# Optimization experiments

Hardware: AMD Instinct MI355X
Metric: run time of the kernel (lower is better)

The kernel has to match this reference:

```python
import jax, jax.numpy as jnp
import numpy as np
from jax import lax

B, T = 128, 512
V, D = 100000, 100   # word vocab, word embedding dim
H = 100              # per-direction LSTM hidden (concat -> 200)
L = 25               # number of CRF labels


def setup_inputs() -> dict:
    key = jax.random.key(0)
    ks = jax.random.split(key, 16)
    s = 0.02
    inp = {
        "tok_tensor": jax.random.randint(ks[0], (B, T), 0, V, dtype=jnp.int32),
        "tag_tensor": jax.random.randint(ks[1], (B, T), 0, L, dtype=jnp.int32),
        "lengths": jnp.full((B,), T, dtype=jnp.int32),
        "word_emb": jax.random.normal(ks[2], (V, D), jnp.float32) * s,
        # forward-direction LSTM (PyTorch gate order i,f,g,o)
        "w_ih_f": jax.random.normal(ks[3], (4 * H, D), jnp.float32) * s,
        "w_hh_f": jax.random.normal(ks[4], (4 * H, H), jnp.float32) * s,
        "b_ih_f": jax.random.normal(ks[5], (4 * H,), jnp.float32) * s,
        "b_hh_f": jax.random.normal(ks[6], (4 * H,), jnp.float32) * s,
        # backward-direction LSTM
        "w_ih_b": jax.random.normal(ks[7], (4 * H, D), jnp.float32) * s,
        "w_hh_b": jax.random.normal(ks[8], (4 * H, H), jnp.float32) * s,
        "b_ih_b": jax.random.normal(ks[9], (4 * H,), jnp.float32) * s,
        "b_hh_b": jax.random.normal(ks[10], (4 * H,), jnp.float32) * s,
        # hidden2tag linear
        "w_tag": jax.random.normal(ks[11], (L, 2 * H), jnp.float32) * s,
        "b_tag": jax.random.normal(ks[12], (L,), jnp.float32) * s,
        # CRF params
        "transitions": jax.random.normal(ks[13], (L, L), jnp.float32) * 0.1,
        "start_trans": jax.random.normal(ks[14], (L,), jnp.float32) * 0.1,
        "end_trans": jax.random.normal(ks[15], (L,), jnp.float32) * 0.1,
    }
    return inp


def _lstm(x_tbd, w_ih, w_hh, b_ih, b_hh, reverse):
    """x_tbd: [T,B,D] -> hidden states [T,B,H], aligned with input time axis."""
    Bh = x_tbd.shape[1]
    Hh = w_hh.shape[1]
    h0 = jnp.zeros((Bh, Hh), x_tbd.dtype)
    c0 = jnp.zeros((Bh, Hh), x_tbd.dtype)

    def step(carry, xt):
        h, c = carry
        gates = xt @ w_ih.T + b_ih + h @ w_hh.T + b_hh
        i, f, g, o = jnp.split(gates, 4, axis=-1)
        i = jax.nn.sigmoid(i); f = jax.nn.sigmoid(f)
        g = jnp.tanh(g); o = jax.nn.sigmoid(o)
        c = f * c + i * g
        h = o * jnp.tanh(c)
        return (h, c), h

    _, hs = lax.scan(step, (h0, c0), x_tbd, reverse=reverse)
    return hs


def _crf_nll(emissions, tags, mask, transitions, start_trans, end_trans):
    """Sum over batch of -(gold path score - log partition).
    emissions: [B,T,L], tags: [B,T] int, mask: [B,T] float (1=valid)."""
    Bb = emissions.shape[0]
    b_idx = jnp.arange(Bb)
    em_t = emissions.transpose(1, 0, 2)   # [T,B,L]
    tags_t = tags.T                       # [T,B]
    mask_t = mask.T                       # [T,B]

    # --- gold path score ---
    first_tags = tags_t[0]
    score0 = start_trans[first_tags] + em_t[0][b_idx, first_tags]

    def num_step(score, inp):
        em, tp, tc, m = inp  # emissions[t], tags[t-1], tags[t], mask[t]
        s = transitions[tp, tc] + em[b_idx, tc]
        return score + m * s, None

    gold, _ = lax.scan(num_step, score0,
                       (em_t[1:], tags_t[:-1], tags_t[1:], mask_t[1:]))
    last_idx = jnp.sum(mask, axis=1).astype(jnp.int32) - 1
    last_tags = tags[b_idx, last_idx]
    gold = gold + end_trans[last_tags]

    # --- log partition (forward algorithm) ---
    alpha0 = start_trans + em_t[0]  # [B,L]

    def part_step(alpha, inp):
        em, m = inp
        # [B,L_prev,1] + [L_prev,L_next] + [B,1,L_next]
        nxt = jax.nn.logsumexp(alpha[:, :, None] + transitions[None] + em[:, None, :], axis=1)
        alpha = jnp.where(m[:, None] > 0, nxt, alpha)
        return alpha, None

    alpha, _ = lax.scan(part_step, alpha0, (em_t[1:], mask_t[1:]))
    logZ = jax.nn.logsumexp(alpha + end_trans, axis=1)
    return jnp.sum(logZ - gold)


def reference(tok_tensor, tag_tensor, lengths,
              word_emb, w_ih_f, w_hh_f, b_ih_f, b_hh_f,
              w_ih_b, w_hh_b, b_ih_b, b_hh_b,
              w_tag, b_tag, transitions, start_trans, end_trans):
    # word embedding lookup: [B,T,D]
    tok_embs = word_emb[tok_tensor]
    x_tbd = tok_embs.transpose(1, 0, 2)  # [T,B,D]
    # BiLSTM encoder (dropout off: eval / deterministic reference)
    h_fwd = _lstm(x_tbd, w_ih_f, w_hh_f, b_ih_f, b_hh_f, reverse=False)
    h_bwd = _lstm(x_tbd, w_ih_b, w_hh_b, b_ih_b, b_hh_b, reverse=True)
    seq = jnp.concatenate([h_fwd, h_bwd], axis=-1).transpose(1, 0, 2)  # [B,T,2H]
    # hidden2tag
    emissions = jnp.einsum('btd,ld->btl', seq, w_tag) + b_tag  # [B,T,L]
    # CRF negative log-likelihood
    mask = (jnp.arange(T)[None, :] < lengths[:, None]).astype(emissions.dtype)
    return _crf_nll(emissions, tag_tensor, mask, transitions, start_trans, end_trans)
```

## Files before the change

kernel.cpp:

```cpp
#include <hip/hip_runtime.h>
#include <cstdint>
#include <cstddef>

#define BB 128
#define TT 512
#define DD 100
#define HH 100
#define NG 400
#define LL 25
#define TS 32
#define NTILE 16
#define F_LOG2E 1.44269504088896340736f
#define F_LN2   0.69314718055994530942f

typedef __decltype(__builtin_amdgcn_cvt_pkrtz(0.f, 0.f)) h2_t;
typedef _Float16 v8h __attribute__((ext_vector_type(8)));
typedef float v4f __attribute__((ext_vector_type(4)));

__device__ __forceinline__ h2_t bc_h2(unsigned int u) {
  return __builtin_bit_cast(h2_t, u);
}
__device__ __forceinline__ unsigned int pk(float x, float y) {
  return __builtin_bit_cast(unsigned int, __builtin_amdgcn_cvt_pkrtz(x, y));
}

__device__ __forceinline__ float fdot2(h2_t a, h2_t b, float c) {
#if __has_builtin(__builtin_amdgcn_fdot2)
  return __builtin_amdgcn_fdot2(a, b, c, false);
#else
  return c + (float)a[0] * (float)b[0] + (float)a[1] * (float)b[1];
#endif
}

__device__ __forceinline__ float fexp2(float x) { return __builtin_amdgcn_exp2f(x); }
__device__ __forceinline__ float flog2(float x) { return __builtin_amdgcn_logf(x); }
__device__ __forceinline__ float frcp(float x)  { return __builtin_amdgcn_rcpf(x); }

__device__ __forceinline__ float sigmoid_f(float x) {
  return frcp(1.f + fexp2(-F_LOG2E * x));
}
__device__ __forceinline__ float tanh_f(float x) {
  float e = fexp2(2.f * F_LOG2E * x);
  return 1.f - 2.f * frcp(e + 1.f);
}

template <int CTRL>
__device__ __forceinline__ float qadd(float v) {
#if __has_builtin(__builtin_amdgcn_mov_dpp)
  int m = __builtin_amdgcn_mov_dpp(__builtin_bit_cast(int, v), CTRL, 0xF, 0xF, true);
  return v + __builtin_bit_cast(float, m);
#else
  int x = (CTRL == 177) ? 1 : 2;
  return v + __shfl_xor(v, x);
#endif
}

template <int LANE>
__device__ __forceinline__ float qbcast(float v) {
#if __has_builtin(__builtin_amdgcn_mov_dpp)
  int m = __builtin_amdgcn_mov_dpp(__builtin_bit_cast(int, v), LANE * 0x55, 0xF, 0xF, true);
  return __builtin_bit_cast(float, m);
#else
  return __shfl(v, (threadIdx.x & 63 & ~3) + LANE);
#endif
}

__device__ __forceinline__ float rfl(float v) {
  return __builtin_bit_cast(float,
      __builtin_amdgcn_readfirstlane(__builtin_bit_cast(int, v)));
}

__device__ __forceinline__ void wave_fence() {
#if __has_builtin(__builtin_amdgcn_wave_barrier)
  __builtin_amdgcn_wave_barrier();
#endif
}

__device__ __forceinline__ void lds_barrier() {
  __builtin_amdgcn_s_waitcnt(0xC07F);
  __builtin_amdgcn_s_barrier();
}

__global__ __launch_bounds__(512, 2) void lstm_fused3(
    const int* __restrict__ tok, const float* __restrict__ emb,
    const float* __restrict__ w_ih_f, const float* __restrict__ w_ih_b,
    const float* __restrict__ b_ih_f, const float* __restrict__ b_hh_f,
    const float* __restrict__ b_ih_b, const float* __restrict__ b_hh_b,
    const float* __restrict__ w_hh_f, const float* __restrict__ w_hh_b,
    const float* __restrict__ w_tag, const float* __restrict__ b_tag,
    float* __restrict__ em_f, float* __restrict__ em_b)
{
  const int tid = threadIdx.x;
  const int b   = blockIdx.x & 127;
  const int dir = blockIdx.x >> 7;
  const float* w_hh = dir ? w_hh_b : w_hh_f;
  const float* w_ih = dir ? w_ih_b : w_ih_f;
  const float* b_ih = dir ? b_ih_b : b_ih_f;
  const float* b_hh = dir ? b_hh_b : b_hh_f;

  __shared__ __align__(16) unsigned short gin_lds[TS * 400];
  __shared__ __align__(16) unsigned int xlds[TS * 68];
  __shared__ __align__(16) unsigned int hls0[52];
  __shared__ __align__(16) unsigned int hls1[52];

  const int wv   = tid >> 6;
  const int lane = tid & 63;
  const int l16  = lane & 15;
  const int quad = lane >> 4;
  const int c0b  = (25 * wv) >> 3;
  const int c1b  = (25 * (wv + 1)) >> 3;
  const int ncol = c1b - c0b;

  v8h bfr[4][4];
  int pcol[4];
#pragma unroll
  for (int ci = 0; ci < 4; ++ci) {
    const int cc = (ci < ncol) ? (c0b + ci) : c0b;
    const int n  = 16 * cc + l16;
    const float* wr = w_ih + (size_t)n * DD;
#pragma unroll
    for (int f = 0; f < 3; ++f) {
      const float* wp = wr + f * 32 + quad * 8;
      float4 va = *(const float4*)(wp);
      float4 vb = *(const float4*)(wp + 4);
      uint4 u;
      u.x = pk(va.x, va.y); u.y = pk(va.z, va.w);
      u.z = pk(vb.x, vb.y); u.w = pk(vb.z, vb.w);
      bfr[ci][f] = __builtin_bit_cast(v8h, u);
    }
    {
      uint4 u = {0u, 0u, 0u, 0u};
      if (quad == 0) {
        float4 va = *(const float4*)(wr + 96);
        u.x = pk(va.x, va.y); u.y = pk(va.z, va.w);
      }
      bfr[ci][3] = __builtin_bit_cast(v8h, u);
    }
    const int qn = (n * 41) >> 12;
    pcol[ci] = ((n - 100 * qn) << 2) + qn;
  }

  for (int i = tid; i < TS * 18; i += 512) {
    int row = i / 18;
    int d = i - row * 18;
    xlds[row * 68 + 50 + d] = 0u;
  }

  const bool uact = tid < NG;
  const int j = tid >> 2;
  const int s = tid & 3;
  const int od = 12 * s;
  const int nnv = (s == 3) ? 14 : 12;

  h2_t wA[14], wB[14], wC[14], wD[14];
  float bias = 0.f;
  if (uact) {
#pragma unroll
    for (int d = 0; d < 14; ++d) {
      int dd = (d < nnv) ? (od + d) : 0;
      const float* r0 = w_hh + (size_t)(0 * 100 + j) * HH + 2 * dd;
      const float* r1 = w_hh + (size_t)(1 * 100 + j) * HH + 2 * dd;
      const float* r2 = w_hh + (size_t)(2 * 100 + j) * HH + 2 * dd;
      const float* r3 = w_hh + (size_t)(3 * 100 + j) * HH + 2 * dd;
      h2_t z = __builtin_amdgcn_cvt_pkrtz(0.f, 0.f);
      wA[d] = (d < nnv) ? __builtin_amdgcn_cvt_pkrtz(r0[0], r0[1]) : z;
      wB[d] = (d < nnv) ? __builtin_amdgcn_cvt_pkrtz(r1[0], r1[1]) : z;
      wC[d] = (d < nnv) ? __builtin_amdgcn_cvt_pkrtz(r2[0], r2[1]) : z;
      wD[d] = (d < nnv) ? __builtin_amdgcn_cvt_pkrtz(r3[0], r3[1]) : z;
    }
    bias = b_ih[s * 100 + j] + b_hh[s * 100 + j];
  }
  const float kk2 = (s == 2) ? (2.f * F_LOG2E) : (-F_LOG2E);
  const float cA  = (s == 2) ? -2.f : 1.f;
  const float cB  = (s == 2) ? 1.f : 0.f;

  const int el = tid - 448;
  const bool eact = (el >= 0) && (el < 50);
  const int l  = (el >= 0) ? (el >> 1) : 0;
  const int hf = (el >= 0) ? (el & 1) : 0;
  const int eo = hf ? 24 : 0;
  const int en = hf ? 26 : 24;
  h2_t wt[26];
  float bt = 0.f;
  if (eact) {
    const float* wr = w_tag + (size_t)l * 200 + dir * 100;
#pragma unroll
    for (int d = 0; d < 26; ++d) {
      int dd = (d < en) ? (eo + d) : 0;
      h2_t z = __builtin_amdgcn_cvt_pkrtz(0.f, 0.f);
      wt[d] = (d < en) ? __builtin_amdgcn_cvt_pkrtz(wr[2 * dd], wr[2 * dd + 1]) : z;
    }
    if (dir == 0 && hf == 0) bt = b_tag[l];
  }
  float* emo = dir ? em_b : em_f;
  float* emp = emo + ((size_t)b * TT + (dir ? (TT - 1) : 0)) * LL + l;
  const ptrdiff_t estep = dir ? -(ptrdiff_t)LL : (ptrdiff_t)LL;

  if (tid < 52) { hls0[tid] = 0u; hls1[tid] = 0u; }

  const int tprow = tid / 13;
  const int tps   = tid - 13 * tprow;
  const bool tp_act = tid < 416;

  float4 xa = {0, 0, 0, 0}, xb = {0, 0, 0, 0};
  if (tp_act) {
    int ii = tprow;
    int tt = dir ? (TT - 1 - ii) : ii;
    int tk = tok[b * TT + tt];
    const float* xp = emb + (size_t)tk * DD + 8 * tps;
    xa = *(const float4*)xp;
    if (tps < 12) xb = *(const float4*)(xp + 4);
  }

  float c = 0.f;
  unsigned short gnext = 0;
  int grow = 0;

#define SDOT(d, hh) \
  p0 = fdot2(wA[d], bc_h2(hh), p0); p1 = fdot2(wB[d], bc_h2(hh), p1); \
  p2 = fdot2(wC[d], bc_h2(hh), p2); p3 = fdot2(wD[d], bc_h2(hh), p3);
#define EDOT(d, hh) { h2_t h = bc_h2(hh); \
  if ((d & 3) == 0) a0 = fdot2(wt[d], h, a0); \
  else if ((d & 3) == 1) a1 = fdot2(wt[d], h, a1); \
  else if ((d & 3) == 2) a2 = fdot2(wt[d], h, a2); \
  else a3 = fdot2(wt[d], h, a3); }

#define SCAN_STEP(HRD, HWR, TVNZ)                                          \
  {                                                                        \
    if (uact) {                                                            \
      unsigned short gcurr = gnext;                                        \
      int nr = (grow < TS - 1) ? grow + 1 : TS - 1;                        \
      gnext = gin_lds[nr * 400 + tid];                                     \
      grow = nr;                                                           \
      const unsigned int* hp = (HRD) + od;                                 \
      uint4 u0 = *((const uint4*)hp);                                      \
      uint4 u1 = *((const uint4*)(hp + 4));                                \
      uint4 u2 = *((const uint4*)(hp + 8));                                \
      uint2 u3 = *((const uint2*)(hp + 12));                               \
      float p0, p1, p2, p3;                                                \
      p0 = fdot2(wA[0], bc_h2(u0.x), 0.f);                                 \
      p1 = fdot2(wB[0], bc_h2(u0.x), 0.f);                                 \
      p2 = fdot2(wC[0], bc_h2(u0.x), 0.f);                                 \
      p3 = fdot2(wD[0], bc_h2(u0.x), 0.f);                                 \
      SDOT(1, u0.y)  SDOT(2, u0.z)  SDOT(3, u0.w)                          \
      SDOT(4, u1.x)  SDOT(5, u1.y)  SDOT(6, u1.z)  SDOT(7, u1.w)           \
      SDOT(8, u2.x)  SDOT(9, u2.y)  SDOT(10, u2.z) SDOT(11, u2.w)          \
      SDOT(12, u3.x) SDOT(13, u3.y)                                        \
      p0 = qadd<78>(qadd<177>(p0));                                        \
      p1 = qadd<78>(qadd<177>(p1));                                        \
      p2 = qadd<78>(qadd<177>(p2));                                        \
      p3 = qadd<78>(qadd<177>(p3));                                        \
      float psel = (s == 0) ? p0 : (s == 1) ? p1 : (s == 2) ? p2 : p3;     \
      float gate = psel + bias + (float)__builtin_bit_cast(__fp16, gcurr); \
      float y  = fexp2(kk2 * gate);                                        \
      float rr = frcp(1.f + y);                                            \
      float actv = fmaf(cA, rr, cB);                                       \
      float iv = qbcast<0>(actv);                                          \
      float fv = qbcast<1>(actv);                                          \
      float gv = qbcast<2>(actv);                                          \
      float ov = qbcast<3>(actv);                                          \
      c = fmaf(fv, c, iv * gv);                                            \
      float hvv = ov * tanh_f(c);                                          \
      if (s == 0) ((__fp16*)(HWR))[j] = (__fp16)hvv;                       \
    } else if (eact && (TVNZ)) {                                           \
      const unsigned int* hp = (HRD) + eo;                                 \
      uint4 e0 = *((const uint4*)hp);                                      \
      uint4 e1 = *((const uint4*)(hp + 4));                                \
      uint4 e2 = *((const uint4*)(hp + 8));                                \
      uint4 e3 = *((const uint4*)(hp + 12));                               \
      uint4 e4 = *((const uint4*)(hp + 16));                               \
      uint4 e5 = *((const uint4*)(hp + 20));                               \
      uint2 e6 = *((const uint2*)(hp + 24));                               \
      float a0, a1, a2, a3;                                                \
      a0 = fdot2(wt[0], bc_h2(e0.x), 0.f);                                 \
      a1 = fdot2(wt[1], bc_h2(e0.y), 0.f);                                 \
      a2 = fdot2(wt[2], bc_h2(e0.z), 0.f);                                 \
      a3 = fdot2(wt[3], bc_h2(e0.w), 0.f);                                 \
      EDOT(4, e1.x)  EDOT(5, e1.y)  EDOT(6, e1.z)  EDOT(7, e1.w)           \
      EDOT(8, e2.x)  EDOT(9, e2.y)  EDOT(10, e2.z) EDOT(11, e2.w)          \
      EDOT(12, e3.x) EDOT(13, e3.y) EDOT(14, e3.z) EDOT(15, e3.w)          \
      EDOT(16, e4.x) EDOT(17, e4.y) EDOT(18, e4.z) EDOT(19, e4.w)          \
      EDOT(20, e5.x) EDOT(21, e5.y) EDOT(22, e5.z) EDOT(23, e5.w)          \
      EDOT(24, e6.x) EDOT(25, e6.y)                                        \
      float ss = (a0 + a1) + (a2 + a3);                                    \
      float tot = qadd<177>(ss);                                           \
      if (hf == 0) *emp = tot + bt;                                        \
      emp += estep;                                                        \
    }                                                                      \
    lds_barrier();                                                         \
  }

  __syncthreads();

  for (int T = 0; T < NTILE; ++T) {
    if (tp_act) {
      unsigned int* xr = xlds + tprow * 68 + 4 * tps;
      if (tps < 12) {
        uint4 u;
        u.x = pk(xa.x, xa.y); u.y = pk(xa.z, xa.w);
        u.z = pk(xb.x, xb.y); u.w = pk(xb.z, xb.w);
        *(uint4*)xr = u;
      } else {
        xr[0] = pk(xa.x, xa.y);
        xr[1] = pk(xa.z, xa.w);
      }
    }
    __syncthreads();

    {
      v8h af[2][4];
#pragma unroll
      for (int rg = 0; rg < 2; ++rg)
#pragma unroll
        for (int f = 0; f < 4; ++f)
          af[rg][f] = __builtin_bit_cast(v8h,
              *(const uint4*)(xlds + (rg * 16 + l16) * 68 + f * 16 + quad * 4));

      if (tp_act && T + 1 < NTILE) {
        int ii = (T + 1) * TS + tprow;
        int tt = dir ? (TT - 1 - ii) : ii;
        int tk = tok[b * TT + tt];
        const float* xp = emb + (size_t)tk * DD + 8 * tps;
        xa = *(const float4*)xp;
        if (tps < 12) xb = *(const float4*)(xp + 4);
      }

      __fp16* gout = (__fp16*)gin_lds;
#pragma unroll
      for (int ci = 0; ci < 4; ++ci) {
        if (ci >= ncol) break;
        const int p = pcol[ci];
#pragma unroll
        for (int rg = 0; rg < 2; ++rg) {
          v4f acc = {0.f, 0.f, 0.f, 0.f};
          acc = __builtin_amdgcn_mfma_f32_16x16x32_f16(af[rg][0], bfr[ci][0], acc, 0, 0, 0);
          acc = __builtin_amdgcn_mfma_f32_16x16x32_f16(af[rg][1], bfr[ci][1], acc, 0, 0, 0);
          acc = __builtin_amdgcn_mfma_f32_16x16x32_f16(af[rg][2], bfr[ci][2], acc, 0, 0, 0);
          acc = __builtin_amdgcn_mfma_f32_16x16x32_f16(af[rg][3], bfr[ci][3], acc, 0, 0, 0);
          const int rowb = rg * 16 + quad * 4;
#pragma unroll
          for (int r = 0; r < 4; ++r)
            gout[(rowb + r) * 400 + p] = (__fp16)acc[r];
        }
      }
    }
    __syncthreads();
    if (uact) { grow = 0; gnext = gin_lds[tid]; }

    SCAN_STEP(hls0, hls1, (T > 0))
    SCAN_STEP(hls1, hls0, true)
    for (int it = 1; it < TS / 2; ++it) {
      SCAN_STEP(hls0, hls1, true)
      SCAN_STEP(hls1, hls0, true)
    }
  }
#undef SCAN_STEP
#undef SDOT

  if (eact) {
    const unsigned int* hp = hls0 + eo;
    uint4 e0 = *((const uint4*)hp);
    uint4 e1 = *((const uint4*)(hp + 4));
    uint4 e2 = *((const uint4*)(hp + 8));
    uint4 e3 = *((const uint4*)(hp + 12));
    uint4 e4 = *((const uint4*)(hp + 16));
    uint4 e5 = *((const uint4*)(hp + 20));
    uint2 e6 = *((const uint2*)(hp + 24));
    float a0, a1, a2, a3;
    a0 = fdot2(wt[0], bc_h2(e0.x), 0.f);
    a1 = fdot2(wt[1], bc_h2(e0.y), 0.f);
    a2 = fdot2(wt[2], bc_h2(e0.z), 0.f);
    a3 = fdot2(wt[3], bc_h2(e0.w), 0.f);
    EDOT(4, e1.x)  EDOT(5, e1.y)  EDOT(6, e1.z)  EDOT(7, e1.w)
    EDOT(8, e2.x)  EDOT(9, e2.y)  EDOT(10, e2.z) EDOT(11, e2.w)
    EDOT(12, e3.x) EDOT(13, e3.y) EDOT(14, e3.z) EDOT(15, e3.w)
    EDOT(16, e4.x) EDOT(17, e4.y) EDOT(18, e4.z) EDOT(19, e4.w)
    EDOT(20, e5.x) EDOT(21, e5.y) EDOT(22, e5.z) EDOT(23, e5.w)
    EDOT(24, e6.x) EDOT(25, e6.y)
    float ss = (a0 + a1) + (a2 + a3);
    float tot = qadd<177>(ss);
    if (hf == 0) {
      int ttp = dir ? 0 : (TT - 1);
      emo[((size_t)b * TT + ttp) * LL + l] = tot + bt;
    }
  }
#undef EDOT
}

#define CHN  8
#define CLEN 64
__device__ __align__(16) float g_PT[(size_t)BB * CHN * LL * 28];

__global__ __launch_bounds__(128, 2) void crf_chunks(
    const float* __restrict__ em_f, const float* __restrict__ em_b,
    const float* __restrict__ trans)
{
  const int tid = threadIdx.x;
  const int b   = blockIdx.x >> 3;
  const int c   = blockIdx.x & 7;
  const int ts  = c * CLEN;

  __shared__ __align__(16) float Al[2][LL][28];
  __shared__ __align__(16) float el[CLEN][32];

  {
    const int row  = tid >> 1;
    const int half = tid & 1;
    const int jb   = half ? 13 : 0;
    const int nj   = half ? 12 : 13;
    const float* pf = em_f + ((size_t)b * TT + ts + row) * LL;
    const float* pb = em_b + ((size_t)b * TT + ts + row) * LL;
    for (int q = 0; q < nj; ++q) {
      int jj = jb + q;
      el[row][jj] = fexp2((pf[jj] + pb[jj]) * F_LOG2E);
    }
  }

  const bool lact = tid < 125;
  const int i  = tid / 5;
  const int jg = tid - 5 * i;
  const int j0 = 5 * jg;

  float E[25][5];
  if (lact) {
#pragma unroll
    for (int k = 0; k < 25; ++k) {
      const float* tr = trans + k * 25 + j0;
#pragma unroll
      for (int u = 0; u < 5; ++u)
        E[k][u] = fexp2(tr[u] * F_LOG2E - 5.f);
    }
#pragma unroll
    for (int u = 0; u < 5; ++u)
      Al[0][i][j0 + u] = (i == j0 + u) ? 1.f : 0.f;
  }
  __syncthreads();

  int p = 0;
  const int s0 = (c == 0) ? 1 : 0;
  for (int st = s0; st < CLEN; ++st) {
    if (lact) {
      const float* ar = &Al[p][i][0];
      float4 q0 = *(const float4*)(ar);
      float4 q1 = *(const float4*)(ar + 4);
      float4 q2 = *(const float4*)(ar + 8);
      float4 q3 = *(const float4*)(ar + 12);
      float4 q4 = *(const float4*)(ar + 16);
      float4 q5 = *(const float4*)(ar + 20);
      float a24 = ar[24];
      float e0 = el[st][j0];
      float e1 = el[st][j0 + 1];
      float e2 = el[st][j0 + 2];
      float e3 = el[st][j0 + 3];
      float e4 = el[st][j0 + 4];
      float av[25] = {q0.x, q0.y, q0.z, q0.w, q1.x, q1.y, q1.z, q1.w,
                      q2.x, q2.y, q2.z, q2.w, q3.x, q3.y, q3.z, q3.w,
                      q4.x, q4.y, q4.z, q4.w, q5.x, q5.y, q5.z, q5.w, a24};
      float c0 = 0.f, c1 = 0.f, c2 = 0.f, c3 = 0.f, c4 = 0.f;
#pragma unroll
      for (int k = 0; k < 25; ++k) {
        float avk = av[k];
        c0 = fmaf(avk, E[k][0], c0);
        c1 = fmaf(avk, E[k][1], c1);
        c2 = fmaf(avk, E[k][2], c2);
        c3 = fmaf(avk, E[k][3], c3);
        c4 = fmaf(avk, E[k][4], c4);
      }
      float* wr = &Al[p ^ 1][i][j0];
      wr[0] = c0 * e0; wr[1] = c1 * e1; wr[2] = c2 * e2;
      wr[3] = c3 * e3; wr[4] = c4 * e4;
    }
    __syncthreads();
    p ^= 1;
  }

  if (lact) {
    const size_t base = ((size_t)(b * CHN + c)) * LL;
#pragma unroll
    for (int u = 0; u < 5; ++u)
      g_PT[(base + (j0 + u)) * 28 + i] = Al[p][i][j0 + u];
  }
}

__global__ __launch_bounds__(128) void crf_combine(
    const float* __restrict__ em_f, const float* __restrict__ em_b,
    const int* __restrict__ tags, const int* __restrict__ lengths,
    const float* __restrict__ trans,
    const float* __restrict__ startt, const float* __restrict__ endt,
    float* __restrict__ out)
{
  const int tid = threadIdx.x;
  const int b   = blockIdx.x;

  __shared__ __align__(16) float Vs[28];

  if (tid < 64) {
    const int lane = tid;
    const int j = (lane < LL) ? lane : 0;
    const float* ef0 = em_f + (size_t)b * TT * LL;
    const float* eb0 = em_b + (size_t)b * TT * LL;
    float v = fexp2((startt[j] + ef0[j] + eb0[j]) * F_LOG2E);
    float C = 0.f;
    for (int c = 0; c < CHN; ++c) {
      if (lane < LL) Vs[lane] = v;
      wave_fence();
      float4 s0 = *(const float4*)(Vs);
      float4 s1 = *(const float4*)(Vs + 4);
      float4 s2 = *(const float4*)(Vs + 8);
      float4 s3 = *(const float4*)(Vs + 12);
      float4 s4 = *(const float4*)(Vs + 16);
      float4 s5 = *(const float4*)(Vs + 20);
      float s24 = Vs[24];
      wave_fence();
      const float* pr = g_PT + ((size_t)(b * CHN + c) * LL + j) * 28;
      float4 p0 = *(const float4*)(pr);
      float4 p1 = *(const float4*)(pr + 4);
      float4 p2 = *(const float4*)(pr + 8);
      float4 p3 = *(const float4*)(pr + 12);
      float4 p4 = *(const float4*)(pr + 16);
      float4 p5 = *(const float4*)(pr + 20);
      float p24 = pr[24];
      float nv = s0.x * p0.x;
      nv = fmaf(s0.y, p0.y, nv); nv = fmaf(s0.z, p0.z, nv); nv = fmaf(s0.w, p0.w, nv);
      nv = fmaf(s1.x, p1.x, nv); nv = fmaf(s1.y, p1.y, nv);
      nv = fmaf(s1.z, p1.z, nv); nv = fmaf(s1.w, p1.w, nv);
      nv = fmaf(s2.x, p2.x, nv); nv = fmaf(s2.y, p2.y, nv);
      nv = fmaf(s2.z, p2.z, nv); nv = fmaf(s2.w, p2.w, nv);
      nv = fmaf(s3.x, p3.x, nv); nv = fmaf(s3.y, p3.y, nv);
      nv = fmaf(s3.z, p3.z, nv); nv = fmaf(s3.w, p3.w, nv);
      nv = fmaf(s4.x, p4.x, nv); nv = fmaf(s4.y, p4.y, nv);
      nv = fmaf(s4.z, p4.z, nv); nv = fmaf(s4.w, p4.w, nv);
      nv = fmaf(s5.x, p5.x, nv); nv = fmaf(s5.y, p5.y, nv);
      nv = fmaf(s5.z, p5.z, nv); nv = fmaf(s5.w, p5.w, nv);
      nv = fmaf(s24, p24, nv);
      float nv0 = rfl(nv);
      int k = ((__builtin_bit_cast(int, nv0) >> 23) & 255) - 127;
      k = (k > 100) ? 100 : ((k < -100) ? -100 : k);
      float scl = __builtin_bit_cast(float, (127 - k) << 23);
      v = nv * scl;
      C += (float)k;
    }
    float term = (lane < LL) ? v * fexp2(endt[j] * F_LOG2E) : 0.f;
    for (int o = 32; o > 0; o >>= 1) term += __shfl_down(term, o);
    if (lane == 0)
      atomicAdd(out, (flog2(term) + C + 5.f * 511.f) * F_LN2);
  } else {
    const int lane = tid & 63;
    const int len = lengths[b];
    float acc = 0.f;
#pragma unroll
    for (int k = 0; k < 8; ++k) {
      int t = k * 64 + lane;
      int tg = tags[b * TT + t];
      size_t ei = ((size_t)b * TT + t) * LL + tg;
      float e = em_f[ei] + em_b[ei];
      float term;
      if (t == 0) term = startt[tg] + e;
      else        term = trans[tags[b * TT + t - 1] * LL + tg] + e;
      if (t == len - 1) term += endt[tg];
      if (t < len) acc += term;
    }
    for (int o = 32; o > 0; o >>= 1) acc += __shfl_down(acc, o);
    if (lane == 0) atomicAdd(out, -acc);
  }
}

extern "C" void kernel_launch(void* const* d_in, const int* in_sizes, int n_in,
                              void* d_out, int out_size, void* d_ws, size_t ws_size,
                              hipStream_t stream) {
  const int*   tok   = (const int*)d_in[0];
  const int*   tags  = (const int*)d_in[1];
  const int*   lens  = (const int*)d_in[2];
  const float* emb   = (const float*)d_in[3];
  const float* wif   = (const float*)d_in[4];
  const float* whf   = (const float*)d_in[5];
  const float* bif   = (const float*)d_in[6];
  const float* bhf   = (const float*)d_in[7];
  const float* wib   = (const float*)d_in[8];
  const float* whb   = (const float*)d_in[9];
  const float* bib   = (const float*)d_in[10];
  const float* bhb   = (const float*)d_in[11];
  const float* wtag  = (const float*)d_in[12];
  const float* btag  = (const float*)d_in[13];
  const float* trans = (const float*)d_in[14];
  const float* st    = (const float*)d_in[15];
  const float* en    = (const float*)d_in[16];

  char* wsb = (char*)d_ws;
  float* em_f = (float*)wsb;
  float* em_b = (float*)(wsb + 6553600);

  hipMemsetAsync(d_out, 0, sizeof(float), stream);

  lstm_fused3<<<256, 512, 0, stream>>>(tok, emb, wif, wib, bif, bhf, bib, bhb,
                                       whf, whb, wtag, btag, em_f, em_b);
  crf_chunks<<<BB * CHN, 128, 0, stream>>>(em_f, em_b, trans);
  crf_combine<<<BB, 128, 0, stream>>>(em_f, em_b, tags, lens, trans, st, en,
                                      (float*)d_out);
}
```

Measured before the change: 426.9 us.

## Defer emission projection to per-tile MFMA GEMM and widen recurrent threads

Per-step emission dot products on separate threads are removed from the scan loop. Each step's hidden state is now stored into an LDS history buffer, and waves 4-7 compute the hidden2tag projection for a whole tile with MFMA after that tile finishes. The recurrent update is remapped from 400 threads (4 per hidden unit, one gate each, quad broadcast) to 200 threads (2 per unit, all four gates each), which cuts cross-lane shuffles but doubles the fdot2 chain per thread. The new layout costs extra LDS and registers.

```diff
diff --git a/kernel.cpp b/kernel.cpp
--- a/kernel.cpp
+++ b/kernel.cpp
@@ -23,6 +23,11 @@
 __device__ __forceinline__ unsigned int pk(float x, float y) {
   return __builtin_bit_cast(unsigned int, __builtin_amdgcn_cvt_pkrtz(x, y));
 }
+__device__ __forceinline__ unsigned int pk_rte(float x, float y) {
+  unsigned short a = __builtin_bit_cast(unsigned short, (__fp16)x);
+  unsigned short c = __builtin_bit_cast(unsigned short, (__fp16)y);
+  return (unsigned int)a | ((unsigned int)c << 16);
+}
 
 __device__ __forceinline__ float fdot2(h2_t a, h2_t b, float c) {
 #if __has_builtin(__builtin_amdgcn_fdot2)
@@ -81,7 +86,7 @@
   __builtin_amdgcn_s_barrier();
 }
 
-__global__ __launch_bounds__(512, 2) void lstm_fused3(
+__global__ __launch_bounds__(512, 2) void lstm_fused4(
     const int* __restrict__ tok, const float* __restrict__ emb,
     const float* __restrict__ w_ih_f, const float* __restrict__ w_ih_b,
     const float* __restrict__ b_ih_f, const float* __restrict__ b_hh_f,
@@ -97,11 +102,13 @@
   const float* w_ih = dir ? w_ih_b : w_ih_f;
   const float* b_ih = dir ? b_ih_b : b_ih_f;
   const float* b_hh = dir ? b_hh_b : b_hh_f;
+  float* emo = dir ? em_b : em_f;
 
   __shared__ __align__(16) unsigned short gin_lds[TS * 400];
   __shared__ __align__(16) unsigned int xlds[TS * 68];
-  __shared__ __align__(16) unsigned int hls0[52];
-  __shared__ __align__(16) unsigned int hls1[52];
+  __shared__ __align__(16) unsigned int hhist[TS * 68];
+  __shared__ __align__(16) unsigned int hls0[56];
+  __shared__ __align__(16) unsigned int hls1[56];
 
   const int wv   = tid >> 6;
   const int lane = tid & 63;
@@ -144,59 +151,69 @@
     int row = i / 18;
     int d = i - row * 18;
     xlds[row * 68 + 50 + d] = 0u;
-  }
-
-  const bool uact = tid < NG;
-  const int j = tid >> 2;
-  const int s = tid & 3;
-  const int od = 12 * s;
-  const int nnv = (s == 3) ? 14 : 12;
-
-  h2_t wA[14], wB[14], wC[14], wD[14];
-  float bias = 0.f;
+    hhist[row * 68 + 50 + d] = 0u;
+  }
+
+  const bool uact = tid < 200;
+  const int j  = tid >> 1;
+  const int s2 = tid & 1;
+
+  h2_t wG0[25], wG1[25], wG2[25], wG3[25];
+  float bias0 = 0.f, bias1 = 0.f, bias2 = 0.f, bias3 = 0.f;
   if (uact) {
-#pragma unroll
-    for (int d = 0; d < 14; ++d) {
-      int dd = (d < nnv) ? (od + d) : 0;
-      const float* r0 = w_hh + (size_t)(0 * 100 + j) * HH + 2 * dd;
-      const float* r1 = w_hh + (size_t)(1 * 100 + j) * HH + 2 * dd;
-      const float* r2 = w_hh + (size_t)(2 * 100 + j) * HH + 2 * dd;
-      const float* r3 = w_hh + (size_t)(3 * 100 + j) * HH + 2 * dd;
-      h2_t z = __builtin_amdgcn_cvt_pkrtz(0.f, 0.f);
-      wA[d] = (d < nnv) ? __builtin_amdgcn_cvt_pkrtz(r0[0], r0[1]) : z;
-      wB[d] = (d < nnv) ? __builtin_amdgcn_cvt_pkrtz(r1[0], r1[1]) : z;
-      wC[d] = (d < nnv) ? __builtin_amdgcn_cvt_pkrtz(r2[0], r2[1]) : z;
-      wD[d] = (d < nnv) ? __builtin_amdgcn_cvt_pkrtz(r3[0], r3[1]) : z;
-    }
-    bias = b_ih[s * 100 + j] + b_hh[s * 100 + j];
-  }
-  const float kk2 = (s == 2) ? (2.f * F_LOG2E) : (-F_LOG2E);
-  const float cA  = (s == 2) ? -2.f : 1.f;
-  const float cB  = (s == 2) ? 1.f : 0.f;
-
-  const int el = tid - 448;
-  const bool eact = (el >= 0) && (el < 50);
-  const int l  = (el >= 0) ? (el >> 1) : 0;
-  const int hf = (el >= 0) ? (el & 1) : 0;
-  const int eo = hf ? 24 : 0;
-  const int en = hf ? 26 : 24;
-  h2_t wt[26];
-  float bt = 0.f;
-  if (eact) {
-    const float* wr = w_tag + (size_t)l * 200 + dir * 100;
-#pragma unroll
-    for (int d = 0; d < 26; ++d) {
-      int dd = (d < en) ? (eo + d) : 0;
-      h2_t z = __builtin_amdgcn_cvt_pkrtz(0.f, 0.f);
-      wt[d] = (d < en) ? __builtin_amdgcn_cvt_pkrtz(wr[2 * dd], wr[2 * dd + 1]) : z;
-    }
-    if (dir == 0 && hf == 0) bt = b_tag[l];
-  }
-  float* emo = dir ? em_b : em_f;
-  float* emp = emo + ((size_t)b * TT + (dir ? (TT - 1) : 0)) * LL + l;
-  const ptrdiff_t estep = dir ? -(ptrdiff_t)LL : (ptrdiff_t)LL;
-
-  if (tid < 52) { hls0[tid] = 0u; hls1[tid] = 0u; }
+    const float* r0 = w_hh + (size_t)(0 * 100 + j) * HH + 50 * s2;
+    const float* r1 = w_hh + (size_t)(1 * 100 + j) * HH + 50 * s2;
+    const float* r2 = w_hh + (size_t)(2 * 100 + j) * HH + 50 * s2;
+    const float* r3 = w_hh + (size_t)(3 * 100 + j) * HH + 50 * s2;
+#pragma unroll
+    for (int d = 0; d < 25; ++d) {
+      float2 v0 = *(const float2*)(r0 + 2 * d);
+      float2 v1 = *(const float2*)(r1 + 2 * d);
+      float2 v2 = *(const float2*)(r2 + 2 * d);
+      float2 v3 = *(const float2*)(r3 + 2 * d);
+      wG0[d] = __builtin_amdgcn_cvt_pkrtz(v0.x, v0.y);
+      wG1[d] = __builtin_amdgcn_cvt_pkrtz(v1.x, v1.y);
+      wG2[d] = __builtin_amdgcn_cvt_pkrtz(v2.x, v2.y);
+      wG3[d] = __builtin_amdgcn_cvt_pkrtz(v3.x, v3.y);
+    }
+    bias0 = b_ih[j]       + b_hh[j];
+    bias1 = b_ih[100 + j] + b_hh[100 + j];
+    bias2 = b_ih[200 + j] + b_hh[200 + j];
+    bias3 = b_ih[300 + j] + b_hh[300 + j];
+  }
+
+  const int ew    = wv - 4;
+  const int ecb   = ew & 1;
+  const int erg   = (ew >> 1) & 1;
+  const int encol = 16 * ecb + l16;
+  const bool eact2 = (wv >= 4) && (encol < LL);
+  v8h etag[4];
+  float ebias = 0.f;
+  if (wv >= 4) {
+#pragma unroll
+    for (int f = 0; f < 3; ++f) {
+      uint4 u = {0u, 0u, 0u, 0u};
+      if (eact2) {
+        const float* wp = w_tag + (size_t)encol * 200 + dir * 100 + f * 32 + quad * 8;
+        float4 va = *(const float4*)(wp);
+        float4 vb = *(const float4*)(wp + 4);
+        u.x = pk(va.x, va.y); u.y = pk(va.z, va.w);
+        u.z = pk(vb.x, vb.y); u.w = pk(vb.z, vb.w);
+      }
+      etag[f] = __builtin_bit_cast(v8h, u);
+    }
+    {
+      uint4 u = {0u, 0u, 0u, 0u};
+      if (eact2 && quad == 0) {
+        float4 va = *(const float4*)(w_tag + (size_t)encol * 200 + dir * 100 + 96);
+        u.x = pk(va.x, va.y); u.y = pk(va.z, va.w);
+      }
+      etag[3] = __builtin_bit_cast(v8h, u);
+    }
+    if (eact2 && dir == 0) ebias = b_tag[encol];
+  }
+
+  if (tid < 56) { hls0[tid] = 0u; hls1[tid] = 0u; }
 
   const int tprow = tid / 13;
   const int tps   = tid - 13 * tprow;
@@ -213,81 +230,78 @@
   }
 
   float c = 0.f;
-  unsigned short gnext = 0;
-  int grow = 0;
-
-#define SDOT(d, hh) \
-  p0 = fdot2(wA[d], bc_h2(hh), p0); p1 = fdot2(wB[d], bc_h2(hh), p1); \
-  p2 = fdot2(wC[d], bc_h2(hh), p2); p3 = fdot2(wD[d], bc_h2(hh), p3);
-#define EDOT(d, hh) { h2_t h = bc_h2(hh); \
-  if ((d & 3) == 0) a0 = fdot2(wt[d], h, a0); \
-  else if ((d & 3) == 1) a1 = fdot2(wt[d], h, a1); \
-  else if ((d & 3) == 2) a2 = fdot2(wt[d], h, a2); \
-  else a3 = fdot2(wt[d], h, a3); }
-
-#define SCAN_STEP(HRD, HWR, TVNZ)                                          \
+  uint2 gnext = {0u, 0u};
+
+#define SD2(d, hw) { h2_t hv = bc_h2(hw);                                  \
+  p0 = fdot2(wG0[d], hv, p0); p1 = fdot2(wG1[d], hv, p1);                  \
+  p2 = fdot2(wG2[d], hv, p2); p3 = fdot2(wG3[d], hv, p3); }
+
+#define SCAN2(HRD, HWR, ROW)                                               \
   {                                                                        \
     if (uact) {                                                            \
-      unsigned short gcurr = gnext;                                        \
-      int nr = (grow < TS - 1) ? grow + 1 : TS - 1;                        \
-      gnext = gin_lds[nr * 400 + tid];                                     \
-      grow = nr;                                                           \
-      const unsigned int* hp = (HRD) + od;                                 \
+      uint2 gcurr = gnext;                                                 \
+      int nr = ((ROW) < TS - 1) ? (ROW) + 1 : TS - 1;                      \
+      gnext = ((const uint2*)(gin_lds + nr * 400))[j];                     \
+      const unsigned int* hp = (HRD) + 28 * s2;                            \
       uint4 u0 = *((const uint4*)hp);                                      \
       uint4 u1 = *((const uint4*)(hp + 4));                                \
       uint4 u2 = *((const uint4*)(hp + 8));                                \
-      uint2 u3 = *((const uint2*)(hp + 12));                               \
-      float p0, p1, p2, p3;                                                \
-      p0 = fdot2(wA[0], bc_h2(u0.x), 0.f);                                 \
-      p1 = fdot2(wB[0], bc_h2(u0.x), 0.f);                                 \
-      p2 = fdot2(wC[0], bc_h2(u0.x), 0.f);                                 \
-      p3 = fdot2(wD[0], bc_h2(u0.x), 0.f);                                 \
-      SDOT(1, u0.y)  SDOT(2, u0.z)  SDOT(3, u0.w)                          \
-      SDOT(4, u1.x)  SDOT(5, u1.y)  SDOT(6, u1.z)  SDOT(7, u1.w)           \
-      SDOT(8, u2.x)  SDOT(9, u2.y)  SDOT(10, u2.z) SDOT(11, u2.w)          \
-      SDOT(12, u3.x) SDOT(13, u3.y)                                        \
-      p0 = qadd<78>(qadd<177>(p0));                                        \
-      p1 = qadd<78>(qadd<177>(p1));                                        \
-      p2 = qadd<78>(qadd<177>(p2));                                        \
-      p3 = qadd<78>(qadd<177>(p3));                                        \
-      float psel = (s == 0) ? p0 : (s == 1) ? p1 : (s == 2) ? p2 : p3;     \
-      float gate = psel + bias + (float)__builtin_bit_cast(__fp16, gcurr); \
-      float y  = fexp2(kk2 * gate);                                        \
-      float rr = frcp(1.f + y);                                            \
-      float actv = fmaf(cA, rr, cB);                                       \
-      float iv = qbcast<0>(actv);                                          \
-      float fv = qbcast<1>(actv);                                          \
-      float gv = qbcast<2>(actv);                                          \
-      float ov = qbcast<3>(actv);                                          \
+      uint4 u3 = *((const uint4*)(hp + 12));                               \
+      uint4 u4 = *((const uint4*)(hp + 16));                               \
+      uint4 u5 = *((const uint4*)(hp + 20));                               \
+      unsigned int u6 = hp[24];                                            \
+      float p0 = 0.f, p1 = 0.f, p2 = 0.f, p3 = 0.f;                        \
+      SD2(0, u0.x)  SD2(1, u0.y)  SD2(2, u0.z)  SD2(3, u0.w)               \
+      SD2(4, u1.x)  SD2(5, u1.y)  SD2(6, u1.z)  SD2(7, u1.w)               \
+      SD2(8, u2.x)  SD2(9, u2.y)  SD2(10, u2.z) SD2(11, u2.w)              \
+      SD2(12, u3.x) SD2(13, u3.y) SD2(14, u3.z) SD2(15, u3.w)              \
+      SD2(16, u4.x) SD2(17, u4.y) SD2(18, u4.z) SD2(19, u4.w)              \
+      SD2(20, u5.x) SD2(21, u5.y) SD2(22, u5.z) SD2(23, u5.w)              \
+      SD2(24, u6)                                                          \
+      p0 = qadd<177>(p0); p1 = qadd<177>(p1);                              \
+      p2 = qadd<177>(p2); p3 = qadd<177>(p3);                              \
+      h2_t glo = bc_h2(gcurr.x), ghi = bc_h2(gcurr.y);                     \
+      float gi = p0 + bias0 + (float)glo[0];                               \
+      float gf = p1 + bias1 + (float)glo[1];                               \
+      float gg = p2 + bias2 + (float)ghi[0];                               \
+      float go = p3 + bias3 + (float)ghi[1];                               \
+      float iv = sigmoid_f(gi);                                            \
+      float fv = sigmoid_f(gf);                                            \
+      float gv = tanh_f(gg);                                               \
+      float ov = sigmoid_f(go);                                            \
       c = fmaf(fv, c, iv * gv);                                            \
       float hvv = ov * tanh_f(c);                                          \
-      if (s == 0) ((__fp16*)(HWR))[j] = (__fp16)hvv;                       \
-    } else if (eact && (TVNZ)) {                                           \
-      const unsigned int* hp = (HRD) + eo;                                 \
-      uint4 e0 = *((const uint4*)hp);                                      \
-      uint4 e1 = *((const uint4*)(hp + 4));                                \
-      uint4 e2 = *((const uint4*)(hp + 8));                                \
-      uint4 e3 = *((const uint4*)(hp + 12));                               \
-      uint4 e4 = *((const uint4*)(hp + 16));                               \
-      uint4 e5 = *((const uint4*)(hp + 20));                               \
-      uint2 e6 = *((const uint2*)(hp + 24));                               \
-      float a0, a1, a2, a3;                                                \
-      a0 = fdot2(wt[0], bc_h2(e0.x), 0.f);                                 \
-      a1 = fdot2(wt[1], bc_h2(e0.y), 0.f);                                 \
-      a2 = fdot2(wt[2], bc_h2(e0.z), 0.f);                                 \
-      a3 = fdot2(wt[3], bc_h2(e0.w), 0.f);                                 \
-      EDOT(4, e1.x)  EDOT(5, e1.y)  EDOT(6, e1.z)  EDOT(7, e1.w)           \
-      EDOT(8, e2.x)  EDOT(9, e2.y)  EDOT(10, e2.z) EDOT(11, e2.w)          \
-      EDOT(12, e3.x) EDOT(13, e3.y) EDOT(14, e3.z) EDOT(15, e3.w)          \
-      EDOT(16, e4.x) EDOT(17, e4.y) EDOT(18, e4.z) EDOT(19, e4.w)          \
-      EDOT(20, e5.x) EDOT(21, e5.y) EDOT(22, e5.z) EDOT(23, e5.w)          \
-      EDOT(24, e6.x) EDOT(25, e6.y)                                        \
-      float ss = (a0 + a1) + (a2 + a3);                                    \
-      float tot = qadd<177>(ss);                                           \
-      if (hf == 0) *emp = tot + bt;                                        \
-      emp += estep;                                                        \
+      float hnb = qbcast<2>(hvv);                                          \
+      if ((tid & 3) == 0) {                                                \
+        int k = tid >> 2;                                                  \
+        unsigned int val = pk_rte(hvv, hnb);                               \
+        (HWR)[k + (k >= 25 ? 3 : 0)] = val;                                \
+        hhist[(ROW) * 68 + k] = val;                                       \
+      }                                                                    \
     }                                                                      \
     lds_barrier();                                                         \
+  }
+
+#define EMIT_GEMM(TB)                                                      \
+  {                                                                        \
+    const unsigned int* hb = hhist + (erg * 16 + l16) * 68 + quad * 4;     \
+    v8h ah0 = __builtin_bit_cast(v8h, *(const uint4*)(hb));                \
+    v8h ah1 = __builtin_bit_cast(v8h, *(const uint4*)(hb + 16));           \
+    v8h ah2 = __builtin_bit_cast(v8h, *(const uint4*)(hb + 32));           \
+    v8h ah3 = __builtin_bit_cast(v8h, *(const uint4*)(hb + 48));           \
+    v4f ea = {0.f, 0.f, 0.f, 0.f};                                         \
+    ea = __builtin_amdgcn_mfma_f32_16x16x32_f16(ah0, etag[0], ea, 0, 0, 0);\
+    ea = __builtin_amdgcn_mfma_f32_16x16x32_f16(ah1, etag[1], ea, 0, 0, 0);\
+    ea = __builtin_amdgcn_mfma_f32_16x16x32_f16(ah2, etag[2], ea, 0, 0, 0);\
+    ea = __builtin_amdgcn_mfma_f32_16x16x32_f16(ah3, etag[3], ea, 0, 0, 0);\
+    if (eact2) {                                                           \
+      const int tb = (TB) + erg * 16 + quad * 4;                           \
+      _Pragma("unroll")                                                    \
+      for (int r = 0; r < 4; ++r) {                                        \
+        int t = dir ? (TT - 1 - (tb + r)) : (tb + r);                      \
+        emo[((size_t)b * TT + t) * LL + encol] = ea[r] + ebias;            \
+      }                                                                    \
+    }                                                                      \
   }
 
   __syncthreads();
@@ -343,48 +357,26 @@
             gout[(rowb + r) * 400 + p] = (__fp16)acc[r];
         }
       }
+
+      if (wv >= 4 && T > 0) {
+        EMIT_GEMM((T - 1) * TS)
+      }
     }
     __syncthreads();
-    if (uact) { grow = 0; gnext = gin_lds[tid]; }
-
-    SCAN_STEP(hls0, hls1, (T > 0))
-    SCAN_STEP(hls1, hls0, true)
-    for (int it = 1; it < TS / 2; ++it) {
-      SCAN_STEP(hls0, hls1, true)
-      SCAN_STEP(hls1, hls0, true)
-    }
-  }
-#undef SCAN_STEP
-#undef SDOT
-
-  if (eact) {
-    const unsigned int* hp = hls0 + eo;
-    uint4 e0 = *((const uint4*)hp);
-    uint4 e1 = *((const uint4*)(hp + 4));
-    uint4 e2 = *((const uint4*)(hp + 8));
-    uint4 e3 = *((const uint4*)(hp + 12));
-    uint4 e4 = *((const uint4*)(hp + 16));
-    uint4 e5 = *((const uint4*)(hp + 20));
-    uint2 e6 = *((const uint2*)(hp + 24));
-    float a0, a1, a2, a3;
-    a0 = fdot2(wt[0], bc_h2(e0.x), 0.f);
-    a1 = fdot2(wt[1], bc_h2(e0.y), 0.f);
-    a2 = fdot2(wt[2], bc_h2(e0.z), 0.f);
-    a3 = fdot2(wt[3], bc_h2(e0.w), 0.f);
-    EDOT(4, e1.x)  EDOT(5, e1.y)  EDOT(6, e1.z)  EDOT(7, e1.w)
-    EDOT(8, e2.x)  EDOT(9, e2.y)  EDOT(10, e2.z) EDOT(11, e2.w)
-    EDOT(12, e3.x) EDOT(13, e3.y) EDOT(14, e3.z) EDOT(15, e3.w)
-    EDOT(16, e4.x) EDOT(17, e4.y) EDOT(18, e4.z) EDOT(19, e4.w)
-    EDOT(20, e5.x) EDOT(21, e5.y) EDOT(22, e5.z) EDOT(23, e5.w)
-    EDOT(24, e6.x) EDOT(25, e6.y)
-    float ss = (a0 + a1) + (a2 + a3);
-    float tot = qadd<177>(ss);
-    if (hf == 0) {
-      int ttp = dir ? 0 : (TT - 1);
-      emo[((size_t)b * TT + ttp) * LL + l] = tot + bt;
-    }
-  }
-#undef EDOT
+    if (uact) gnext = ((const uint2*)gin_lds)[j];
+
+    for (int it = 0; it < TS; it += 2) {
+      SCAN2(hls0, hls1, it)
+      SCAN2(hls1, hls0, it + 1)
+    }
+  }
+
+  if (wv >= 4) {
+    EMIT_GEMM((NTILE - 1) * TS)
+  }
+#undef EMIT_GEMM
+#undef SCAN2
+#undef SD2
 }
 
 #define CHN  8
@@ -592,7 +584,7 @@
 
   hipMemsetAsync(d_out, 0, sizeof(float), stream);
 
-  lstm_fused3<<<256, 512, 0, stream>>>(tok, emb, wif, wib, bif, bhf, bib, bhb,
+  lstm_fused4<<<256, 512, 0, stream>>>(tok, emb, wif, wib, bif, bhf, bib, bhb,
                                        whf, whb, wtag, btag, em_f, em_b);
   crf_chunks<<<BB * CHN, 128, 0, stream>>>(em_f, em_b, trans);
   crf_combine<<<BB, 128, 0, stream>>>(em_f, em_b, tags, lens, trans, st, en,
```

After: 410.7 us. 3.8% less time.
